# Kernel tuning notes

Measured on AMD Instinct MI355X. Metric: run time of the kernel, lower is better.

Reference implementation:

```python
import jax, jax.numpy as jnp
import numpy as np

H = 512          # hidden_size
F = 2048         # intermediate_size
E = 16           # n_routed_experts
SHARED = 2       # n_shared_experts
TOP_K = 4        # n_activated_experts
B, S = 2, 2048


def _mlp(x, w1, b1, w2, b2):
    # Standard MLP: Linear -> GELU(exact) -> Linear (dropout inactive at eval)
    return jax.nn.gelu(x @ w1 + b1, approximate=False) @ w2 + b2


def setup_inputs() -> dict:
    key = jax.random.key(0)
    ks = jax.random.split(key, 10)
    sc = 0.02
    return {
        "hidden_states": jax.random.normal(ks[0], (B, S, H), dtype=jnp.float32),
        "gate_w": jax.random.normal(ks[1], (E, H), dtype=jnp.float32) * sc,  # nn.Linear weight [out,in], no bias
        "re_w1": jax.random.normal(ks[2], (E, H, F), dtype=jnp.float32) * sc,
        "re_b1": jnp.zeros((E, F), dtype=jnp.float32),
        "re_w2": jax.random.normal(ks[3], (E, F, H), dtype=jnp.float32) * sc,
        "re_b2": jnp.zeros((E, H), dtype=jnp.float32),
        "se_w1": jax.random.normal(ks[4], (SHARED, H, F), dtype=jnp.float32) * sc,
        "se_b1": jnp.zeros((SHARED, F), dtype=jnp.float32),
        "se_w2": jax.random.normal(ks[5], (SHARED, F, H), dtype=jnp.float32) * sc,
        "se_b2": jnp.zeros((SHARED, H), dtype=jnp.float32),
    }


def reference(hidden_states, gate_w, re_w1, re_b1, re_w2, re_b2,
              se_w1, se_b1, se_w2, se_b2):
    b, s, h = hidden_states.shape
    x = hidden_states.reshape(-1, h)                       # [T, H]
    # --- gating: softmax -> top-k -> renormalize over top-k ---
    gate_probs = jax.nn.softmax(x @ gate_w.T, axis=-1)     # [T, E]
    top_v, top_i = jax.lax.top_k(gate_probs, TOP_K)        # [T, K]
    top_v = jax.nn.softmax(top_v, axis=-1)
    # combine weights per expert: zero for non-selected experts (same math as masked scatter-add)
    combine = jnp.einsum('tk,tke->te', top_v,
                         jax.nn.one_hot(top_i, E, dtype=x.dtype))  # [T, E]
    # --- routed experts (weight is 0 for tokens not routed to expert e) ---
    routed = jnp.zeros_like(x)
    for e in range(E):
        routed = routed + combine[:, e:e + 1] * _mlp(x, re_w1[e], re_b1[e], re_w2[e], re_b2[e])
    # --- shared experts: average ---
    shared = jnp.zeros_like(x)
    for j in range(SHARED):
        shared = shared + _mlp(x, se_w1[j], se_b1[j], se_w2[j], se_b2[j])
    shared = shared / SHARED
    return (routed + shared).reshape(b, s, h)
```

## Files before the change

kernel.cpp:

```cpp
#include <hip/hip_runtime.h>

#define T_TOK 4096
#define H_DIM 512
#define F_DIM 2048
#define N_EXP 16
#define N_SH  2
#define TOPK  4

typedef __attribute__((ext_vector_type(4))) float f32x4;
typedef __attribute__((ext_vector_type(8))) short bf16x8;

__device__ __forceinline__ unsigned short f2bf(float f){
  union { float f; unsigned u; } a; a.f = f;
  unsigned u = a.u;
  return (unsigned short)((u + 0x7fffu + ((u >> 16) & 1u)) >> 16);
}

__device__ __forceinline__ float fast_gelu(float v){
  float u = 0.7978845608f * (v + 0.044715f * v * v * v);
  u = fminf(fmaxf(u, -15.f), 15.f);
  float e = __expf(2.f * u);
  float th = (e - 1.f) * __builtin_amdgcn_rcpf(e + 1.f);
  return 0.5f * v * (1.f + th);
}

#define GLD16(gsrc, ldst) \
  __builtin_amdgcn_global_load_lds((const __attribute__((address_space(1))) unsigned int*)(gsrc), \
                                   (__attribute__((address_space(3))) unsigned int*)(ldst), 16, 0, 0)

__global__ void moe_transpose2(const float* __restrict__ s0, const float* __restrict__ s1,
                               unsigned short* __restrict__ d0, unsigned short* __restrict__ d1,
                               int R, int C){
  __shared__ float tile[64][65];
  int z = blockIdx.z;
  size_t per = (size_t)R * C;
  const float* src      = (z < N_EXP) ? s0 + (size_t)z * per : s1 + (size_t)(z - N_EXP) * per;
  unsigned short* dst   = (z < N_EXP) ? d0 + (size_t)z * per : d1 + (size_t)(z - N_EXP) * per;
  int c0 = blockIdx.x * 64, r0 = blockIdx.y * 64;
  int t = threadIdx.x;
  #pragma unroll
  for (int i = 0; i < 16; ++i){
    int idx = i * 256 + t; int r = idx >> 6, c = idx & 63;
    tile[r][c] = src[(size_t)(r0 + r) * C + (c0 + c)];
  }
  __syncthreads();
  #pragma unroll
  for (int i = 0; i < 16; ++i){
    int idx = i * 256 + t; int r = idx >> 6, c = idx & 63;
    dst[(size_t)(c0 + r) * R + (r0 + c)] = f2bf(tile[c][r]);
  }
}

__global__ __launch_bounds__(256) void moe_gate(
    const float* __restrict__ x, const float* __restrict__ gw,
    unsigned short* __restrict__ xb,
    int* __restrict__ tki, float* __restrict__ tkw,
    int* __restrict__ counts){
  __shared__ float gwl[N_EXP * H_DIM];
  int tid = threadIdx.x;
  #pragma unroll
  for (int i = 0; i < N_EXP * H_DIM / 256; ++i)
    gwl[i * 256 + tid] = gw[i * 256 + tid];
  __syncthreads();

  int t = blockIdx.x * 256 + tid;
  const float4* xr = (const float4*)(x + (size_t)t * H_DIM);
  ushort4* xw = (ushort4*)(xb + (size_t)t * H_DIM);
  float acc[N_EXP];
  #pragma unroll
  for (int e = 0; e < N_EXP; ++e) acc[e] = 0.f;
  for (int h4 = 0; h4 < H_DIM / 4; ++h4){
    float4 xv = xr[h4];
    ushort4 o; o.x = f2bf(xv.x); o.y = f2bf(xv.y); o.z = f2bf(xv.z); o.w = f2bf(xv.w);
    xw[h4] = o;
    #pragma unroll
    for (int e = 0; e < N_EXP; ++e){
      const float* wrow = &gwl[e * H_DIM + h4 * 4];
      acc[e] += xv.x * wrow[0] + xv.y * wrow[1] + xv.z * wrow[2] + xv.w * wrow[3];
    }
  }
  float m = -1e30f;
  #pragma unroll
  for (int e = 0; e < N_EXP; ++e) m = fmaxf(m, acc[e]);
  float Z = 0.f;
  #pragma unroll
  for (int e = 0; e < N_EXP; ++e){ acc[e] = __expf(acc[e] - m); Z += acc[e]; }
  float inv = 1.f / Z;
  #pragma unroll
  for (int e = 0; e < N_EXP; ++e) acc[e] *= inv;
  int sel[TOPK]; float sv[TOPK];
  unsigned used = 0;
  #pragma unroll
  for (int k = 0; k < TOPK; ++k){
    int best = 0; float bv = -1.f;
    #pragma unroll
    for (int e = 0; e < N_EXP; ++e)
      if (!((used >> e) & 1u) && acc[e] > bv){ bv = acc[e]; best = e; }
    used |= 1u << best; sel[k] = best; sv[k] = bv;
  }
  float m0 = sv[0];
  float Z2 = 0.f;
  #pragma unroll
  for (int k = 0; k < TOPK; ++k){ sv[k] = __expf(sv[k] - m0); Z2 += sv[k]; }
  float i2 = 1.f / Z2;
  #pragma unroll
  for (int k = 0; k < TOPK; ++k){
    tki[t * TOPK + k] = sel[k];
    tkw[t * TOPK + k] = sv[k] * i2;
    atomicAdd(&counts[sel[k]], 1);
  }
}

__global__ void moe_offsets(const int* __restrict__ counts, int* __restrict__ offs,
                            int* __restrict__ cursor){
  if (threadIdx.x == 0){
    int a = 0;
    for (int e = 0; e < N_EXP; ++e){ offs[e] = a; cursor[e] = a; a += counts[e]; }
  }
}

__global__ void moe_build_rows(const int* __restrict__ tki, const float* __restrict__ tkw,
                               int* __restrict__ cursor, int* __restrict__ rows,
                               float* __restrict__ roww){
  int t = blockIdx.x * 256 + threadIdx.x;
  if (t >= T_TOK) return;
  for (int k = 0; k < TOPK; ++k){
    int e = tki[t * TOPK + k];
    int pos = atomicAdd(&cursor[e], 1);
    rows[pos] = t;
    roww[pos] = tkw[t * TOPK + k];
  }
}

__global__ __launch_bounds__(256, 4) void moe_gemm1(
    const unsigned short* __restrict__ xb,
    const unsigned short* __restrict__ rw1T,
    const unsigned short* __restrict__ sw1T,
    const float* __restrict__ rb1, const float* __restrict__ sb1,
    const int* __restrict__ counts, const int* __restrict__ offs,
    const int* __restrict__ rows,
    unsigned short* __restrict__ h_rout, unsigned short* __restrict__ h_sh){
  constexpr int K  = H_DIM;
  constexpr int NK = K / 64;
  int job = blockIdx.z;
  int M; const int* rmap; const unsigned short* wT; const float* bias; unsigned short* hout;
  if (job < N_EXP){
    M = counts[job];
    int base = offs[job];
    rmap = rows + base;
    wT = rw1T + (size_t)job * F_DIM * H_DIM;
    bias = rb1 + job * F_DIM;
    hout = h_rout + (size_t)base * F_DIM;
  } else {
    int s = job - N_EXP;
    M = T_TOK; rmap = nullptr;
    wT = sw1T + (size_t)s * F_DIM * H_DIM;
    bias = sb1 + s * F_DIM;
    hout = h_sh + (size_t)s * T_TOK * F_DIM;
  }
  int m0 = blockIdx.y * 128;
  if (m0 >= M) return;
  int n0 = blockIdx.x * 128;

  __shared__ char smem[32768];
  int tid = threadIdx.x;
  int wave = tid >> 6, lane = tid & 63;
  int wm = wave >> 1, wn = wave & 1;

  const unsigned short* asrc[4];
  const unsigned short* bsrc[4];
  int srow = tid >> 3;
  int slot = tid & 7;
  #pragma unroll
  for (int r = 0; r < 4; ++r){
    int row = r * 32 + srow;
    int gr = m0 + row; if (gr > M - 1) gr = M - 1;
    int tok = rmap ? rmap[gr] : gr;
    asrc[r] = xb + (size_t)tok * H_DIM + ((slot ^ (row & 7)) << 3);
    bsrc[r] = wT + (size_t)(n0 + row) * K + ((slot ^ (row & 7)) << 3);
  }

  f32x4 acc[4][4];
  #pragma unroll
  for (int i = 0; i < 4; ++i)
    #pragma unroll
    for (int j = 0; j < 4; ++j) acc[i][j] = (f32x4)0.f;

  auto stage = [&](int k0){
    #pragma unroll
    for (int r = 0; r < 4; ++r) GLD16(asrc[r] + k0, smem + r * 4096 + wave * 1024);
    #pragma unroll
    for (int r = 0; r < 4; ++r) GLD16(bsrc[r] + k0, smem + 16384 + r * 4096 + wave * 1024);
  };

  for (int kt = 0; kt < NK; ++kt){
    if (kt) __syncthreads();
    stage(kt * 64);
    __syncthreads();
    const char* A = smem;
    const char* B = A + 16384;
    #pragma unroll
    for (int ks = 0; ks < 2; ++ks){
      int kg = ks * 4 + (lane >> 4);
      bf16x8 a[4], b[4];
      #pragma unroll
      for (int f = 0; f < 4; ++f){
        int row = wm * 64 + f * 16 + (lane & 15);
        a[f] = *(const bf16x8*)(A + row * 128 + ((kg ^ (row & 7)) << 4));
      }
      #pragma unroll
      for (int f = 0; f < 4; ++f){
        int row = wn * 64 + f * 16 + (lane & 15);
        b[f] = *(const bf16x8*)(B + row * 128 + ((kg ^ (row & 7)) << 4));
      }
      #pragma unroll
      for (int fm = 0; fm < 4; ++fm)
        #pragma unroll
        for (int fn = 0; fn < 4; ++fn)
          acc[fm][fn] = __builtin_amdgcn_mfma_f32_16x16x32_bf16(a[fm], b[fn], acc[fm][fn], 0, 0, 0);
    }
  }

  #pragma unroll
  for (int fm = 0; fm < 4; ++fm){
    #pragma unroll
    for (int j = 0; j < 4; ++j){
      int row = wm * 64 + fm * 16 + (lane >> 4) * 4 + j;
      int gr = m0 + row;
      if (gr < M){
        #pragma unroll
        for (int fn = 0; fn < 4; ++fn){
          int col = n0 + wn * 64 + fn * 16 + (lane & 15);
          float v = acc[fm][fn][j] + bias[col];
          hout[(size_t)gr * F_DIM + col] = f2bf(fast_gelu(v));
        }
      }
    }
  }
}

__global__ __launch_bounds__(256, 4) void moe_gemm2(
    const unsigned short* __restrict__ h_rout,
    const unsigned short* __restrict__ h_sh,
    const unsigned short* __restrict__ rw2T,
    const unsigned short* __restrict__ sw2T,
    const float* __restrict__ rb2, const float* __restrict__ sb2,
    const int* __restrict__ counts, const int* __restrict__ offs,
    const int* __restrict__ rows, const float* __restrict__ roww,
    float* __restrict__ out){
  constexpr int K  = F_DIM;
  constexpr int NK = K / 64;
  int job = blockIdx.z;
  int M; const unsigned short* aseg; const unsigned short* wT; const float* bias;
  const int* rmap; const float* rwt;
  if (job < N_EXP){
    M = counts[job];
    int base = offs[job];
    aseg = h_rout + (size_t)base * F_DIM;
    rmap = rows + base; rwt = roww + base;
    wT = rw2T + (size_t)job * H_DIM * F_DIM;
    bias = rb2 + job * H_DIM;
  } else {
    int s = job - N_EXP; M = T_TOK;
    aseg = h_sh + (size_t)s * T_TOK * F_DIM;
    rmap = nullptr; rwt = nullptr;
    wT = sw2T + (size_t)s * H_DIM * F_DIM;
    bias = sb2 + s * H_DIM;
  }
  int m0 = blockIdx.y * 128;
  if (m0 >= M) return;
  int n0 = blockIdx.x * 128;

  __shared__ char smem[32768];
  int tid = threadIdx.x;
  int wave = tid >> 6, lane = tid & 63;
  int wm = wave >> 1, wn = wave & 1;

  const unsigned short* asrc[4];
  const unsigned short* bsrc[4];
  int srow = tid >> 3;
  int slot = tid & 7;
  #pragma unroll
  for (int r = 0; r < 4; ++r){
    int row = r * 32 + srow;
    int gr = m0 + row; if (gr > M - 1) gr = M - 1;
    asrc[r] = aseg + (size_t)gr * K + ((slot ^ (row & 7)) << 3);
    bsrc[r] = wT + (size_t)(n0 + row) * K + ((slot ^ (row & 7)) << 3);
  }

  f32x4 acc[4][4];
  #pragma unroll
  for (int i = 0; i < 4; ++i)
    #pragma unroll
    for (int j = 0; j < 4; ++j) acc[i][j] = (f32x4)0.f;

  auto stage = [&](int k0){
    #pragma unroll
    for (int r = 0; r < 4; ++r) GLD16(asrc[r] + k0, smem + r * 4096 + wave * 1024);
    #pragma unroll
    for (int r = 0; r < 4; ++r) GLD16(bsrc[r] + k0, smem + 16384 + r * 4096 + wave * 1024);
  };

  for (int kt = 0; kt < NK; ++kt){
    if (kt) __syncthreads();
    stage(kt * 64);
    __syncthreads();
    const char* A = smem;
    const char* B = A + 16384;
    #pragma unroll
    for (int ks = 0; ks < 2; ++ks){
      int kg = ks * 4 + (lane >> 4);
      bf16x8 a[4], b[4];
      #pragma unroll
      for (int f = 0; f < 4; ++f){
        int row = wm * 64 + f * 16 + (lane & 15);
        a[f] = *(const bf16x8*)(A + row * 128 + ((kg ^ (row & 7)) << 4));
      }
      #pragma unroll
      for (int f = 0; f < 4; ++f){
        int row = wn * 64 + f * 16 + (lane & 15);
        b[f] = *(const bf16x8*)(B + row * 128 + ((kg ^ (row & 7)) << 4));
      }
      #pragma unroll
      for (int fm = 0; fm < 4; ++fm)
        #pragma unroll
        for (int fn = 0; fn < 4; ++fn)
          acc[fm][fn] = __builtin_amdgcn_mfma_f32_16x16x32_bf16(a[fm], b[fn], acc[fm][fn], 0, 0, 0);
    }
  }

  #pragma unroll
  for (int fm = 0; fm < 4; ++fm){
    #pragma unroll
    for (int j = 0; j < 4; ++j){
      int row = wm * 64 + fm * 16 + (lane >> 4) * 4 + j;
      int gr = m0 + row;
      if (gr < M){
        int tok; float coef;
        if (rmap){ tok = rmap[gr]; coef = rwt[gr]; }
        else     { tok = gr;       coef = 1.0f / N_SH; }
        #pragma unroll
        for (int fn = 0; fn < 4; ++fn){
          int col = n0 + wn * 64 + fn * 16 + (lane & 15);
          float v = (acc[fm][fn][j] + bias[col]) * coef;
          atomicAdd(&out[(size_t)tok * H_DIM + col], v);
        }
      }
    }
  }
}

extern "C" void kernel_launch(void* const* d_in, const int* in_sizes, int n_in,
                              void* d_out, int out_size, void* d_ws, size_t ws_size,
                              hipStream_t stream){
  const float* x   = (const float*)d_in[0];
  const float* gw  = (const float*)d_in[1];
  const float* rw1 = (const float*)d_in[2];
  const float* rb1 = (const float*)d_in[3];
  const float* rw2 = (const float*)d_in[4];
  const float* rb2 = (const float*)d_in[5];
  const float* sw1 = (const float*)d_in[6];
  const float* sb1 = (const float*)d_in[7];
  const float* sw2 = (const float*)d_in[8];
  const float* sb2 = (const float*)d_in[9];
  float* out = (float*)d_out;

  char* ws = (char*)d_ws;
  size_t off = 0;
  auto alloc = [&](size_t b){ size_t r = off; off += (b + 255) & ~(size_t)255; return r; };
  unsigned short* xb     = (unsigned short*)(ws + alloc((size_t)T_TOK * H_DIM * 2));
  unsigned short* rw1T   = (unsigned short*)(ws + alloc((size_t)N_EXP * H_DIM * F_DIM * 2));
  unsigned short* rw2T   = (unsigned short*)(ws + alloc((size_t)N_EXP * H_DIM * F_DIM * 2));
  unsigned short* sw1T   = (unsigned short*)(ws + alloc((size_t)N_SH * H_DIM * F_DIM * 2));
  unsigned short* sw2T   = (unsigned short*)(ws + alloc((size_t)N_SH * H_DIM * F_DIM * 2));
  unsigned short* h_rout = (unsigned short*)(ws + alloc((size_t)T_TOK * TOPK * F_DIM * 2));
  unsigned short* h_sh   = (unsigned short*)(ws + alloc((size_t)N_SH * T_TOK * F_DIM * 2));
  int*   counts = (int*)(ws + alloc(64));
  int*   offs   = (int*)(ws + alloc(64));
  int*   cursor = (int*)(ws + alloc(64));
  int*   tki    = (int*)(ws + alloc((size_t)T_TOK * TOPK * 4));
  float* tkw    = (float*)(ws + alloc((size_t)T_TOK * TOPK * 4));
  int*   rowsl  = (int*)(ws + alloc((size_t)T_TOK * TOPK * 4));
  float* roww   = (float*)(ws + alloc((size_t)T_TOK * TOPK * 4));

  hipMemsetAsync(counts, 0, 64, stream);
  hipMemsetAsync(out, 0, (size_t)T_TOK * H_DIM * 4, stream);

  moe_gate<<<T_TOK / 256, 256, 0, stream>>>(x, gw, xb, tki, tkw, counts);

  moe_transpose2<<<dim3(F_DIM / 64, H_DIM / 64, N_EXP + N_SH), 256, 0, stream>>>(
      rw1, sw1, rw1T, sw1T, H_DIM, F_DIM);
  moe_transpose2<<<dim3(H_DIM / 64, F_DIM / 64, N_EXP + N_SH), 256, 0, stream>>>(
      rw2, sw2, rw2T, sw2T, F_DIM, H_DIM);

  moe_offsets<<<1, 64, 0, stream>>>(counts, offs, cursor);
  moe_build_rows<<<T_TOK / 256, 256, 0, stream>>>(tki, tkw, cursor, rowsl, roww);

  moe_gemm1<<<dim3(F_DIM / 128, T_TOK / 128, N_EXP + N_SH), 256, 0, stream>>>(
      xb, rw1T, sw1T, rb1, sb1, counts, offs, rowsl, h_rout, h_sh);
  moe_gemm2<<<dim3(H_DIM / 128, T_TOK / 128, N_EXP + N_SH), 256, 0, stream>>>(
      h_rout, h_sh, rw2T, sw2T, rb2, sb2, counts, offs, rowsl, roww, out);
}
```

Baseline: 542.3 us.

## Split gate dot products across four lanes and remap GEMM grids XCD-aware

The gate kernel now assigns four threads per token, each covering a quarter of the hidden dimension, and combines the partial sums with shuffles. Gate weights are staged in padded shared memory so each thread can read them as float4. This launches four times as many gate blocks, to raise parallelism in a kernel that previously ran only 16 blocks. Both expert GEMMs switch to a flat 1D grid whose block index is remapped so that each of the 8 XCDs receives a contiguous range of tiles, which is meant to improve L2 reuse of weight and activation tiles.

```diff
diff --git a/kernel.cpp b/kernel.cpp
--- a/kernel.cpp
+++ b/kernel.cpp
@@ -56,58 +56,68 @@
     unsigned short* __restrict__ xb,
     int* __restrict__ tki, float* __restrict__ tkw,
     int* __restrict__ counts){
-  __shared__ float gwl[N_EXP * H_DIM];
+  __shared__ float gwl[64 * 132];
   int tid = threadIdx.x;
   #pragma unroll
-  for (int i = 0; i < N_EXP * H_DIM / 256; ++i)
-    gwl[i * 256 + tid] = gw[i * 256 + tid];
+  for (int j = 0; j < 32; ++j){
+    int s = j * 256 + tid;
+    gwl[(s >> 7) * 132 + (s & 127)] = gw[s];
+  }
   __syncthreads();
 
-  int t = blockIdx.x * 256 + tid;
-  const float4* xr = (const float4*)(x + (size_t)t * H_DIM);
-  ushort4* xw = (ushort4*)(xb + (size_t)t * H_DIM);
+  int t = blockIdx.x * 64 + (tid >> 2);
+  int q = tid & 3;
+  const float4* xr = (const float4*)(x  + (size_t)t * H_DIM + q * 128);
+  ushort4*      xw = (ushort4*)     (xb + (size_t)t * H_DIM + q * 128);
   float acc[N_EXP];
   #pragma unroll
   for (int e = 0; e < N_EXP; ++e) acc[e] = 0.f;
-  for (int h4 = 0; h4 < H_DIM / 4; ++h4){
-    float4 xv = xr[h4];
+  for (int i = 0; i < 32; ++i){
+    float4 xv = xr[i];
     ushort4 o; o.x = f2bf(xv.x); o.y = f2bf(xv.y); o.z = f2bf(xv.z); o.w = f2bf(xv.w);
-    xw[h4] = o;
+    xw[i] = o;
     #pragma unroll
     for (int e = 0; e < N_EXP; ++e){
-      const float* wrow = &gwl[e * H_DIM + h4 * 4];
-      acc[e] += xv.x * wrow[0] + xv.y * wrow[1] + xv.z * wrow[2] + xv.w * wrow[3];
-    }
-  }
-  float m = -1e30f;
-  #pragma unroll
-  for (int e = 0; e < N_EXP; ++e) m = fmaxf(m, acc[e]);
-  float Z = 0.f;
-  #pragma unroll
-  for (int e = 0; e < N_EXP; ++e){ acc[e] = __expf(acc[e] - m); Z += acc[e]; }
-  float inv = 1.f / Z;
-  #pragma unroll
-  for (int e = 0; e < N_EXP; ++e) acc[e] *= inv;
-  int sel[TOPK]; float sv[TOPK];
-  unsigned used = 0;
-  #pragma unroll
-  for (int k = 0; k < TOPK; ++k){
-    int best = 0; float bv = -1.f;
-    #pragma unroll
-    for (int e = 0; e < N_EXP; ++e)
-      if (!((used >> e) & 1u) && acc[e] > bv){ bv = acc[e]; best = e; }
-    used |= 1u << best; sel[k] = best; sv[k] = bv;
-  }
-  float m0 = sv[0];
-  float Z2 = 0.f;
-  #pragma unroll
-  for (int k = 0; k < TOPK; ++k){ sv[k] = __expf(sv[k] - m0); Z2 += sv[k]; }
-  float i2 = 1.f / Z2;
-  #pragma unroll
-  for (int k = 0; k < TOPK; ++k){
-    tki[t * TOPK + k] = sel[k];
-    tkw[t * TOPK + k] = sv[k] * i2;
-    atomicAdd(&counts[sel[k]], 1);
+      float4 wv = *(const float4*)&gwl[((e << 2) + q) * 132 + (i << 2)];
+      acc[e] += xv.x * wv.x + xv.y * wv.y + xv.z * wv.z + xv.w * wv.w;
+    }
+  }
+  #pragma unroll
+  for (int e = 0; e < N_EXP; ++e){
+    acc[e] += __shfl_xor(acc[e], 1);
+    acc[e] += __shfl_xor(acc[e], 2);
+  }
+  if (q == 0){
+    float m = -1e30f;
+    #pragma unroll
+    for (int e = 0; e < N_EXP; ++e) m = fmaxf(m, acc[e]);
+    float Z = 0.f;
+    #pragma unroll
+    for (int e = 0; e < N_EXP; ++e){ acc[e] = __expf(acc[e] - m); Z += acc[e]; }
+    float inv = 1.f / Z;
+    #pragma unroll
+    for (int e = 0; e < N_EXP; ++e) acc[e] *= inv;
+    int sel[TOPK]; float sv[TOPK];
+    unsigned used = 0;
+    #pragma unroll
+    for (int k = 0; k < TOPK; ++k){
+      int best = 0; float bv = -1.f;
+      #pragma unroll
+      for (int e = 0; e < N_EXP; ++e)
+        if (!((used >> e) & 1u) && acc[e] > bv){ bv = acc[e]; best = e; }
+      used |= 1u << best; sel[k] = best; sv[k] = bv;
+    }
+    float m0 = sv[0];
+    float Z2 = 0.f;
+    #pragma unroll
+    for (int k = 0; k < TOPK; ++k){ sv[k] = __expf(sv[k] - m0); Z2 += sv[k]; }
+    float i2 = 1.f / Z2;
+    #pragma unroll
+    for (int k = 0; k < TOPK; ++k){
+      tki[t * TOPK + k] = sel[k];
+      tkw[t * TOPK + k] = sv[k] * i2;
+      atomicAdd(&counts[sel[k]], 1);
+    }
   }
 }
 
@@ -142,7 +152,12 @@
     unsigned short* __restrict__ h_rout, unsigned short* __restrict__ h_sh){
   constexpr int K  = H_DIM;
   constexpr int NK = K / 64;
-  int job = blockIdx.z;
+  constexpr int CPX = (18 * 32 * 16) / 8;
+  int L = (blockIdx.x & 7) * CPX + (blockIdx.x >> 3);
+  int n  = L & 15;
+  int mi = (L >> 4) & 31;
+  int job = L >> 9;
+
   int M; const int* rmap; const unsigned short* wT; const float* bias; unsigned short* hout;
   if (job < N_EXP){
     M = counts[job];
@@ -158,9 +173,9 @@
     bias = sb1 + s * F_DIM;
     hout = h_sh + (size_t)s * T_TOK * F_DIM;
   }
-  int m0 = blockIdx.y * 128;
+  int m0 = mi * 128;
   if (m0 >= M) return;
-  int n0 = blockIdx.x * 128;
+  int n0 = n * 128;
 
   __shared__ char smem[32768];
   int tid = threadIdx.x;
@@ -250,7 +265,12 @@
     float* __restrict__ out){
   constexpr int K  = F_DIM;
   constexpr int NK = K / 64;
-  int job = blockIdx.z;
+  constexpr int CPX = (18 * 32 * 4) / 8;
+  int L = (blockIdx.x & 7) * CPX + (blockIdx.x >> 3);
+  int n  = L & 3;
+  int mi = (L >> 2) & 31;
+  int job = L >> 7;
+
   int M; const unsigned short* aseg; const unsigned short* wT; const float* bias;
   const int* rmap; const float* rwt;
   if (job < N_EXP){
@@ -267,9 +287,9 @@
     wT = sw2T + (size_t)s * H_DIM * F_DIM;
     bias = sb2 + s * H_DIM;
   }
-  int m0 = blockIdx.y * 128;
+  int m0 = mi * 128;
   if (m0 >= M) return;
-  int n0 = blockIdx.x * 128;
+  int n0 = n * 128;
 
   __shared__ char smem[32768];
   int tid = threadIdx.x;
@@ -386,7 +406,7 @@
   hipMemsetAsync(counts, 0, 64, stream);
   hipMemsetAsync(out, 0, (size_t)T_TOK * H_DIM * 4, stream);
 
-  moe_gate<<<T_TOK / 256, 256, 0, stream>>>(x, gw, xb, tki, tkw, counts);
+  moe_gate<<<T_TOK / 64, 256, 0, stream>>>(x, gw, xb, tki, tkw, counts);
 
   moe_transpose2<<<dim3(F_DIM / 64, H_DIM / 64, N_EXP + N_SH), 256, 0, stream>>>(
       rw1, sw1, rw1T, sw1T, H_DIM, F_DIM);
@@ -396,8 +416,8 @@
   moe_offsets<<<1, 64, 0, stream>>>(counts, offs, cursor);
   moe_build_rows<<<T_TOK / 256, 256, 0, stream>>>(tki, tkw, cursor, rowsl, roww);
 
-  moe_gemm1<<<dim3(F_DIM / 128, T_TOK / 128, N_EXP + N_SH), 256, 0, stream>>>(
+  moe_gemm1<<<18 * 32 * 16, 256, 0, stream>>>(
       xb, rw1T, sw1T, rb1, sb1, counts, offs, rowsl, h_rout, h_sh);
-  moe_gemm2<<<dim3(H_DIM / 128, T_TOK / 128, N_EXP + N_SH), 256, 0, stream>>>(
+  moe_gemm2<<<18 * 32 * 4, 256, 0, stream>>>(
       h_rout, h_sh, rw2T, sw2T, rb2, sb2, counts, offs, rowsl, roww, out);
 }
```

Measured after the change: 630.7 us. 16.3% more time.
